# Kernel tuning notes

Hardware: AMD Instinct MI355X
Metric: run time of the kernel (lower is better)

## Reference

```python
import jax, jax.numpy as jnp
import numpy as np

B, V, C, H, W, N = 2, 5, 32, 256, 320, 40000


def setup_inputs() -> dict:
    key = jax.random.key(0)
    k1, k2, k3, k4 = jax.random.split(key, 4)
    feature_maps = jax.random.normal(k1, (B, V, C, H, W), dtype=jnp.float32)
    # points with z in [1,4] and normalized image coords mostly inside the frustum
    z = jax.random.uniform(k2, (B, N), minval=1.0, maxval=4.0)
    xn = jax.random.uniform(k3, (B, N), minval=-0.55, maxval=0.55)
    yn = jax.random.uniform(k4, (B, N), minval=-0.45, maxval=0.45)
    pts = jnp.stack([xn * z, yn * z, z], axis=1)  # [B, 3, N]
    f = float(W)
    K = jnp.array([[f, 0.0, W / 2.0], [0.0, f, H / 2.0], [0.0, 0.0, 1.0]], jnp.float32)
    cam_intrinsics = jnp.broadcast_to(K, (B, V, 3, 3)).astype(jnp.float32)
    E = jnp.concatenate([jnp.eye(3, dtype=jnp.float32), jnp.zeros((3, 1), jnp.float32)], axis=1)
    cam_extrinsics = jnp.broadcast_to(E, (B, V, 3, 4)).astype(jnp.float32)
    return {"feature_maps": feature_maps, "pts": pts,
            "cam_intrinsics": cam_intrinsics, "cam_extrinsics": cam_extrinsics}


def _bilinear(fm_flat, gx, gy):
    """grid_sample, mode='bilinear', padding_mode='zeros', align_corners=False.
    fm_flat: [BV, C, H*W]; gx, gy: [BV, N] in [-1, 1]. Returns [BV, C, N]."""
    ix = ((gx + 1.0) * W - 1.0) * 0.5
    iy = ((gy + 1.0) * H - 1.0) * 0.5
    x0 = jnp.floor(ix)
    y0 = jnp.floor(iy)
    wx = ix - x0
    wy = iy - y0
    x0i = x0.astype(jnp.int32)
    y0i = y0.astype(jnp.int32)
    out = jnp.zeros((fm_flat.shape[0], fm_flat.shape[1], gx.shape[1]), fm_flat.dtype)
    corners = ((0, 0, (1.0 - wx) * (1.0 - wy)), (1, 0, wx * (1.0 - wy)),
               (0, 1, (1.0 - wx) * wy), (1, 1, wx * wy))
    for dx, dy, w in corners:
        xc = x0i + dx
        yc = y0i + dy
        valid = (xc >= 0) & (xc < W) & (yc >= 0) & (yc < H)
        idx = jnp.clip(yc, 0, H - 1) * W + jnp.clip(xc, 0, W - 1)  # [BV, N]
        v = jnp.take_along_axis(fm_flat, idx[:, None, :], axis=2)  # [BV, C, N]
        out = out + v * (w * valid)[:, None, :]
    return out


def _forward(feature_maps, pts, cam_intrinsics, cam_extrinsics):
    BV = B * V
    fm = feature_maps.reshape(BV, C, H, W)
    Km = cam_intrinsics.reshape(BV, 3, 3)
    Em = cam_extrinsics.reshape(BV, 3, 4)
    R = Em[:, :, :3]
    t = Em[:, :, 3:]
    pe = jnp.broadcast_to(pts[:, None], (B, V, 3, N)).reshape(BV, 3, N)
    tp = (R @ pe + t).transpose(0, 2, 1)  # [BV, N, 3] camera-space points
    x, y, z = tp[..., 0], tp[..., 1], tp[..., 2]
    nuv = jnp.stack([x / z, y / z, jnp.ones_like(x)], axis=-1)  # [BV, N, 3]
    uv = jnp.einsum('bnj,bij->bni', nuv, Km)[..., :2]  # pixel coords
    gx = (uv[..., 0] - 0.5) / (W - 1) * 2.0 - 1.0
    gy = (uv[..., 1] - 0.5) / (H - 1) * 2.0 - 1.0
    dx = 2.0 / (W - 1)
    dy = 2.0 / (H - 1)
    fm_flat = fm.reshape(BV, C, H * W)
    feat = _bilinear(fm_flat, gx, gy)
    fl = _bilinear(fm_flat, gx - dx, gy)
    fr = _bilinear(fm_flat, gx + dx, gy)
    ft = _bilinear(fm_flat, gx, gy - dy)
    fb = _bilinear(fm_flat, gx, gy + dy)
    grad_x = 0.5 * (fr - fl)
    grad_y = 0.5 * (fb - ft)
    pts_feature = feat.reshape(B, V, C, N)
    pts_feature_grad = jnp.stack([grad_x, grad_y], axis=-1).reshape(B, V, C, N, 2)
    return pts_feature, pts_feature_grad


def reference(feature_maps, pts, cam_intrinsics, cam_extrinsics):
    return _forward(feature_maps, pts, cam_intrinsics, cam_extrinsics)
```

## Files before the change

kernel.cpp:

```cpp
#include <hip/hip_runtime.h>

#define Bc 2
#define Vc 5
#define Cc 32
#define Hc 256
#define Wc 320
#define Nc 40000
#define HWc (Hc * Wc)

typedef float v2f __attribute__((ext_vector_type(2)));

__device__ __forceinline__ unsigned bf16_rn(float x) {
    unsigned u = __float_as_uint(x);
    return (u + 0x7fffu + ((u >> 16) & 1u)) >> 16;
}

__global__ void __launch_bounds__(256)
transpose_bf16_kernel(const float* __restrict__ fm, unsigned short* __restrict__ fmT)
{
    __shared__ float tile[Cc][65];
    const int bv  = blockIdx.y;
    const int hw0 = blockIdx.x * 64;
    const int t   = threadIdx.x;

    const int tx = t & 63;
    const int ty = t >> 6;
    const float* src = fm + (size_t)bv * Cc * HWc + hw0;
    #pragma unroll
    for (int i = 0; i < 8; ++i) {
        int c = ty * 8 + i;
        tile[c][tx] = __builtin_nontemporal_load(&src[(size_t)c * HWc + tx]);
    }
    __syncthreads();

    const int cq = t & 3;
    const int hw = t >> 2;
    unsigned r[4];
    #pragma unroll
    for (int j = 0; j < 4; ++j) {
        float a = tile[cq * 8 + 2 * j][hw];
        float b = tile[cq * 8 + 2 * j + 1][hw];
        r[j] = bf16_rn(a) | (bf16_rn(b) << 16);
    }
    uint4* dst = (uint4*)(fmT + ((size_t)bv * HWc + hw0 + hw) * Cc) + cq;
    *dst = make_uint4(r[0], r[1], r[2], r[3]);
}

__device__ __forceinline__ void corner_setup(float ix, float iy, float coef,
                                             float wk[4], int pix[4])
{
    float x0f = floorf(ix), y0f = floorf(iy);
    float wx = ix - x0f, wy = iy - y0f;
    int x0 = (int)x0f, y0 = (int)y0f;
    float wg0 = (1.0f - wx) * (1.0f - wy);
    float wg1 = wx * (1.0f - wy);
    float wg2 = (1.0f - wx) * wy;
    float wg3 = wx * wy;
    float wg[4] = {wg0, wg1, wg2, wg3};
    #pragma unroll
    for (int k = 0; k < 4; ++k) {
        int xc = x0 + (k & 1);
        int yc = y0 + (k >> 1);
        bool valid = (xc >= 0) & (xc < Wc) & (yc >= 0) & (yc < Hc);
        wk[k] = valid ? coef * wg[k] : 0.0f;
        int xcl = min(max(xc, 0), Wc - 1);
        int ycl = min(max(yc, 0), Hc - 1);
        pix[k] = ycl * Wc + xcl;
    }
}

__global__ void __launch_bounds__(256)
fgf_main(const unsigned short* __restrict__ fmT,
         const float* __restrict__ pts,
         const float* __restrict__ Kmat,
         const float* __restrict__ Emat,
         float* __restrict__ out_feat,
         float* __restrict__ out_grad)
{
    int idx = blockIdx.x * 256 + threadIdx.x;
    int cq = idx & 3;
    int pn = idx >> 2;
    int n  = pn % Nc;
    int bv = pn / Nc;
    int b  = bv / Vc;

    const float* p = pts + (size_t)(b * 3) * Nc + n;
    float px = p[0];
    float py = p[Nc];
    float pz = p[2 * Nc];

    const float* Ep = Emat + bv * 12;
    const float* Kp = Kmat + bv * 9;
    float x = Ep[0] * px + Ep[1] * py + Ep[2]  * pz + Ep[3];
    float y = Ep[4] * px + Ep[5] * py + Ep[6]  * pz + Ep[7];
    float z = Ep[8] * px + Ep[9] * py + Ep[10] * pz + Ep[11];
    float xz = x / z;
    float yz = y / z;
    float u = Kp[0] * xz + Kp[1] * yz + Kp[2];
    float v = Kp[3] * xz + Kp[4] * yz + Kp[5];

    const float sxp = (float)Wc / (float)(Wc - 1);
    const float syp = (float)Hc / (float)(Hc - 1);
    float ix = (u - 0.5f) * sxp - 0.5f;
    float iy = (v - 0.5f) * syp - 0.5f;

    const uint4* base4 = (const uint4*)(fmT + (size_t)bv * HWc * Cc) + cq;

    const float ox[5] = {0.0f, -sxp, sxp, 0.0f, 0.0f};
    const float oy[5] = {0.0f, 0.0f, 0.0f, -syp, syp};
    const float cf[5] = {1.0f, -0.5f, 0.5f, -0.5f, 0.5f};
    const int   as[5] = {0, 1, 1, 2, 2};

    float acc[3][8];
    #pragma unroll
    for (int a = 0; a < 3; ++a)
        #pragma unroll
        for (int j = 0; j < 8; ++j) acc[a][j] = 0.0f;

    float wk[2][4];
    int   pix[2][4];
    uint4 rg[2][4];

    corner_setup(ix + ox[0], iy + oy[0], cf[0], wk[0], pix[0]);
    #pragma unroll
    for (int k = 0; k < 4; ++k) rg[0][k] = base4[(size_t)pix[0][k] * 4];

    #pragma unroll
    for (int s = 0; s < 5; ++s) {
        int cur = s & 1;
        if (s < 4) {
            int nxt = cur ^ 1;
            corner_setup(ix + ox[s + 1], iy + oy[s + 1], cf[s + 1], wk[nxt], pix[nxt]);
            #pragma unroll
            for (int k = 0; k < 4; ++k) rg[nxt][k] = base4[(size_t)pix[nxt][k] * 4];
        }
        float* a = acc[as[s]];
        #pragma unroll
        for (int k = 0; k < 4; ++k) {
            uint4 w = rg[cur][k];
            float ww = wk[cur][k];
            a[0] = fmaf(ww, __uint_as_float(w.x << 16),          a[0]);
            a[1] = fmaf(ww, __uint_as_float(w.x & 0xffff0000u), a[1]);
            a[2] = fmaf(ww, __uint_as_float(w.y << 16),          a[2]);
            a[3] = fmaf(ww, __uint_as_float(w.y & 0xffff0000u), a[3]);
            a[4] = fmaf(ww, __uint_as_float(w.z << 16),          a[4]);
            a[5] = fmaf(ww, __uint_as_float(w.z & 0xffff0000u), a[5]);
            a[6] = fmaf(ww, __uint_as_float(w.w << 16),          a[6]);
            a[7] = fmaf(ww, __uint_as_float(w.w & 0xffff0000u), a[7]);
        }
    }

    size_t obase = (size_t)bv * Cc * Nc + n;
    v2f* gp = (v2f*)out_grad;
    #pragma unroll
    for (int j = 0; j < 8; ++j) {
        int c = cq * 8 + j;
        __builtin_nontemporal_store(acc[0][j], &out_feat[obase + (size_t)c * Nc]);
        v2f g = {acc[1][j], acc[2][j]};
        __builtin_nontemporal_store(g, &gp[obase + (size_t)c * Nc]);
    }
}

__device__ __forceinline__ float fetch_px(const float* __restrict__ fm, int x, int y) {
    if (x < 0 || x >= Wc || y < 0 || y >= Hc) return 0.0f;
    return fm[y * Wc + x];
}
__device__ __forceinline__ float bilin(const float* __restrict__ fm, float ix, float iy) {
    float x0f = floorf(ix), y0f = floorf(iy);
    float wx = ix - x0f, wy = iy - y0f;
    int x0 = (int)x0f, y0 = (int)y0f;
    float v00 = fetch_px(fm, x0, y0);
    float v10 = fetch_px(fm, x0 + 1, y0);
    float v01 = fetch_px(fm, x0, y0 + 1);
    float v11 = fetch_px(fm, x0 + 1, y0 + 1);
    return (v00 * (1.0f - wx) + v10 * wx) * (1.0f - wy)
         + (v01 * (1.0f - wx) + v11 * wx) * wy;
}
__global__ void __launch_bounds__(256)
fgf_fallback(const float* __restrict__ fm,
             const float* __restrict__ pts,
             const float* __restrict__ Kmat,
             const float* __restrict__ Emat,
             float* __restrict__ out_feat,
             float* __restrict__ out_grad)
{
    int idx = blockIdx.x * 256 + threadIdx.x;
    const int total = Bc * Vc * Cc * Nc;
    if (idx >= total) return;
    int n = idx % Nc;
    int tcb = idx / Nc;
    int c = tcb % Cc;
    int bv = tcb / Cc;
    int b = bv / Vc;
    const float* p = pts + (size_t)(b * 3) * Nc + n;
    float px = p[0], py = p[Nc], pz = p[2 * Nc];
    const float* Ep = Emat + bv * 12;
    const float* Kp = Kmat + bv * 9;
    float x = Ep[0] * px + Ep[1] * py + Ep[2] * pz + Ep[3];
    float y = Ep[4] * px + Ep[5] * py + Ep[6] * pz + Ep[7];
    float z = Ep[8] * px + Ep[9] * py + Ep[10] * pz + Ep[11];
    float xz = x / z, yz = y / z;
    float u = Kp[0] * xz + Kp[1] * yz + Kp[2];
    float v = Kp[3] * xz + Kp[4] * yz + Kp[5];
    const float sxp = (float)Wc / (float)(Wc - 1);
    const float syp = (float)Hc / (float)(Hc - 1);
    float ix = (u - 0.5f) * sxp - 0.5f;
    float iy = (v - 0.5f) * syp - 0.5f;
    const float* f = fm + (size_t)(bv * Cc + c) * HWc;
    float feat = bilin(f, ix, iy);
    float fl = bilin(f, ix - sxp, iy);
    float fr = bilin(f, ix + sxp, iy);
    float ft = bilin(f, ix, iy - syp);
    float fb = bilin(f, ix, iy + syp);
    size_t o = (size_t)(bv * Cc + c) * HWc / HWc * 0 + (size_t)(bv * Cc + c) * Nc + n;
    out_feat[o] = feat;
    ((float2*)out_grad)[o] = make_float2(0.5f * (fr - fl), 0.5f * (fb - ft));
}

extern "C" void kernel_launch(void* const* d_in, const int* in_sizes, int n_in,
                              void* d_out, int out_size, void* d_ws, size_t ws_size,
                              hipStream_t stream) {
    const float* fm  = (const float*)d_in[0];
    const float* pts = (const float*)d_in[1];
    const float* K   = (const float*)d_in[2];
    const float* E   = (const float*)d_in[3];

    float* out_feat = (float*)d_out;
    float* out_grad = (float*)d_out + (size_t)Bc * Vc * Cc * Nc;

    const size_t fmT_bytes = (size_t)Bc * Vc * Cc * HWc * sizeof(unsigned short);

    if (ws_size >= fmT_bytes) {
        unsigned short* fmT = (unsigned short*)d_ws;
        dim3 tgrid(HWc / 64, Bc * Vc);
        transpose_bf16_kernel<<<tgrid, 256, 0, stream>>>(fm, fmT);
        const int total = Bc * Vc * Nc * 4;
        fgf_main<<<total / 256, 256, 0, stream>>>(fmT, pts, K, E, out_feat, out_grad);
    } else {
        const int total = Bc * Vc * Cc * Nc;
        fgf_fallback<<<(total + 255) / 256, 256, 0, stream>>>(fm, pts, K, E, out_feat, out_grad);
    }
}
```

Baseline: 277.5 us.

## Split bf16 feature layout into channel halves and remap blocks per XCD

The transposed bf16 feature map is stored as two 16-channel halves per view, each pixel taking 32 bytes instead of 64. The sampling kernel maps each thread to a half and a channel pair, so one warp's gathers touch a smaller footprint. Block IDs are remapped so each XCD gets a contiguous range of work, aiming for better L2 locality on the gathered rows. Index math shifts to 32-bit unsigned offsets. The cost is two passes over the point set per view, one for each channel half.

```diff
diff --git a/kernel.cpp b/kernel.cpp
--- a/kernel.cpp
+++ b/kernel.cpp
@@ -42,7 +42,10 @@
         float b = tile[cq * 8 + 2 * j + 1][hw];
         r[j] = bf16_rn(a) | (bf16_rn(b) << 16);
     }
-    uint4* dst = (uint4*)(fmT + ((size_t)bv * HWc + hw0 + hw) * Cc) + cq;
+    const int half = cq >> 1;
+    const int sub  = cq & 1;
+    uint4* dst = (uint4*)fmT
+               + ((size_t)(bv * 2 + half) * HWc + (hw0 + hw)) * 2 + sub;
     *dst = make_uint4(r[0], r[1], r[2], r[3]);
 }
 
@@ -69,6 +72,10 @@
     }
 }
 
+#define NBLK 6250
+#define XQ   781
+#define XR   2
+
 __global__ void __launch_bounds__(256)
 fgf_main(const unsigned short* __restrict__ fmT,
          const float* __restrict__ pts,
@@ -77,12 +84,20 @@
          float* __restrict__ out_feat,
          float* __restrict__ out_grad)
 {
-    int idx = blockIdx.x * 256 + threadIdx.x;
-    int cq = idx & 3;
-    int pn = idx >> 2;
-    int n  = pn % Nc;
-    int bv = pn / Nc;
-    int b  = bv / Vc;
+    const int b0  = blockIdx.x;
+    const int xcd = b0 & 7;
+    const int i   = b0 >> 3;
+    const int vb  = (xcd < XR) ? xcd * (XQ + 1) + i
+                               : XR * (XQ + 1) + (xcd - XR) * XQ + i;
+
+    const int v    = vb * 256 + (int)threadIdx.x;
+    const int cq2  = v & 1;
+    const int rest = v >> 1;
+    const int n    = rest % Nc;
+    const int bvh  = rest / Nc;
+    const int bv   = bvh >> 1;
+    const int half = bvh & 1;
+    const int b    = bv / Vc;
 
     const float* p = pts + (size_t)(b * 3) * Nc + n;
     float px = p[0];
@@ -97,14 +112,14 @@
     float xz = x / z;
     float yz = y / z;
     float u = Kp[0] * xz + Kp[1] * yz + Kp[2];
-    float v = Kp[3] * xz + Kp[4] * yz + Kp[5];
+    float vv = Kp[3] * xz + Kp[4] * yz + Kp[5];
 
     const float sxp = (float)Wc / (float)(Wc - 1);
     const float syp = (float)Hc / (float)(Hc - 1);
-    float ix = (u - 0.5f) * sxp - 0.5f;
-    float iy = (v - 0.5f) * syp - 0.5f;
-
-    const uint4* base4 = (const uint4*)(fmT + (size_t)bv * HWc * Cc) + cq;
+    float ix = (u  - 0.5f) * sxp - 0.5f;
+    float iy = (vv - 0.5f) * syp - 0.5f;
+
+    const uint4* base4 = (const uint4*)fmT + (size_t)bvh * (HWc * 2) + cq2;
 
     const float ox[5] = {0.0f, -sxp, sxp, 0.0f, 0.0f};
     const float oy[5] = {0.0f, 0.0f, 0.0f, -syp, syp};
@@ -123,7 +138,7 @@
 
     corner_setup(ix + ox[0], iy + oy[0], cf[0], wk[0], pix[0]);
     #pragma unroll
-    for (int k = 0; k < 4; ++k) rg[0][k] = base4[(size_t)pix[0][k] * 4];
+    for (int k = 0; k < 4; ++k) rg[0][k] = base4[(unsigned)pix[0][k] * 2u];
 
     #pragma unroll
     for (int s = 0; s < 5; ++s) {
@@ -132,7 +147,7 @@
             int nxt = cur ^ 1;
             corner_setup(ix + ox[s + 1], iy + oy[s + 1], cf[s + 1], wk[nxt], pix[nxt]);
             #pragma unroll
-            for (int k = 0; k < 4; ++k) rg[nxt][k] = base4[(size_t)pix[nxt][k] * 4];
+            for (int k = 0; k < 4; ++k) rg[nxt][k] = base4[(unsigned)pix[nxt][k] * 2u];
         }
         float* a = acc[as[s]];
         #pragma unroll
@@ -150,11 +165,12 @@
         }
     }
 
+    const int cbase = half * 16 + cq2 * 8;
     size_t obase = (size_t)bv * Cc * Nc + n;
     v2f* gp = (v2f*)out_grad;
     #pragma unroll
     for (int j = 0; j < 8; ++j) {
-        int c = cq * 8 + j;
+        int c = cbase + j;
         __builtin_nontemporal_store(acc[0][j], &out_feat[obase + (size_t)c * Nc]);
         v2f g = {acc[1][j], acc[2][j]};
         __builtin_nontemporal_store(g, &gp[obase + (size_t)c * Nc]);
@@ -212,7 +228,7 @@
     float fr = bilin(f, ix + sxp, iy);
     float ft = bilin(f, ix, iy - syp);
     float fb = bilin(f, ix, iy + syp);
-    size_t o = (size_t)(bv * Cc + c) * HWc / HWc * 0 + (size_t)(bv * Cc + c) * Nc + n;
+    size_t o = (size_t)(bv * Cc + c) * Nc + n;
     out_feat[o] = feat;
     ((float2*)out_grad)[o] = make_float2(0.5f * (fr - fl), 0.5f * (fb - ft));
 }
@@ -234,8 +250,7 @@
         unsigned short* fmT = (unsigned short*)d_ws;
         dim3 tgrid(HWc / 64, Bc * Vc);
         transpose_bf16_kernel<<<tgrid, 256, 0, stream>>>(fm, fmT);
-        const int total = Bc * Vc * Nc * 4;
-        fgf_main<<<total / 256, 256, 0, stream>>>(fmT, pts, K, E, out_feat, out_grad);
+        fgf_main<<<NBLK, 256, 0, stream>>>(fmT, pts, K, E, out_feat, out_grad);
     } else {
         const int total = Bc * Vc * Cc * Nc;
         fgf_fallback<<<(total + 255) / 256, 256, 0, stream>>>(fm, pts, K, E, out_feat, out_grad);
```

Result: no change. 273.5 us (-1.4%).
